# Kernel optimization log

Hardware: AMD Instinct MI355X
Metric: run time of the kernel (lower is better)

Reference implementation:

```python
import jax, jax.numpy as jnp
import numpy as np

NUM_GROUPS = 32
EPS = 1e-5


def group_norm(x, weight, bias):
    # x: (B, C, H, W, D); normalize per (group, spatial) per sample
    b, c, h, w, d = x.shape
    g = NUM_GROUPS
    xg = x.reshape(b, g, c // g, h, w, d)
    mean = xg.mean(axis=(2, 3, 4, 5), keepdims=True)
    var = xg.var(axis=(2, 3, 4, 5), keepdims=True)
    xg = (xg - mean) * jax.lax.rsqrt(var + EPS)
    xn = xg.reshape(b, c, h, w, d)
    return xn * weight[None, :, None, None, None] + bias[None, :, None, None, None]


def setup_inputs() -> dict:
    key = jax.random.key(0)
    ks = jax.random.split(key, 7)
    B, C, H, W, D = 4, 128, 16, 16, 16
    x = jax.random.normal(ks[0], (B, C, H, W, D), dtype=jnp.float32)
    gn_w = jnp.ones((C,), dtype=jnp.float32)
    gn_b = jnp.zeros((C,), dtype=jnp.float32)
    s = 1.0 / np.sqrt(C)
    qkv_w = jax.random.uniform(ks[1], (3 * C, C), minval=-s, maxval=s, dtype=jnp.float32)
    qkv_b = jax.random.uniform(ks[2], (3 * C,), minval=-s, maxval=s, dtype=jnp.float32)
    out_w = jax.random.uniform(ks[3], (C, C), minval=-s, maxval=s, dtype=jnp.float32)
    out_b = jax.random.uniform(ks[4], (C,), minval=-s, maxval=s, dtype=jnp.float32)
    return {"x": x, "gn_w": gn_w, "gn_b": gn_b, "qkv_w": qkv_w,
            "qkv_b": qkv_b, "out_w": out_w, "out_b": out_b}


def reference(x, gn_w, gn_b, qkv_w, qkv_b, out_w, out_b):
    b, c, h, w, d = x.shape
    n = h * w * d
    xn = group_norm(x, gn_w, gn_b)
    # 1x1x1 conv == pointwise linear over channels
    qkv = jnp.einsum('bchwd,oc->bohwd', xn, qkv_w) + qkv_b[None, :, None, None, None]
    q, k, v = jnp.split(qkv, 3, axis=1)
    q = q.transpose(0, 2, 3, 4, 1).reshape(b, n, c)   # (b, n, c)
    k = k.reshape(b, c, n)                             # (b, c, n)
    v = v.transpose(0, 2, 3, 4, 1).reshape(b, n, c)   # (b, n, c)
    scores = jnp.einsum('bnc,bcm->bnm', q, k) * (c ** -0.5)
    attn = jax.nn.softmax(scores, axis=-1)
    out = jnp.einsum('bnm,bmc->bnc', attn, v)          # (b, n, c)
    out = out.reshape(b, h, w, d, c).transpose(0, 4, 1, 2, 3)
    out = jnp.einsum('bchwd,oc->bohwd', out, out_w) + out_b[None, :, None, None, None]
    return out + x
```

## Files before the change

kernel.cpp:

```cpp
#include <hip/hip_runtime.h>

typedef unsigned short u16;
typedef __attribute__((ext_vector_type(8))) short bf16x8;
typedef __attribute__((ext_vector_type(4))) float f32x4;

__device__ __forceinline__ u16 f2bf(float f) {
    union { float f; unsigned u; } v; v.f = f;
    unsigned r = v.u + 0x7fffu + ((v.u >> 16) & 1u);
    return (u16)(r >> 16);
}

__device__ __forceinline__ void gload16(const u16* g, char* l) {
    __builtin_amdgcn_global_load_lds(
        (const __attribute__((address_space(1))) unsigned int*)g,
        (__attribute__((address_space(3))) unsigned int*)l, 16, 0, 0);
}

__global__ __launch_bounds__(256)
void k_stats(const float* __restrict__ x, float* __restrict__ mean, float* __restrict__ rstd)
{
    int bg = blockIdx.x, t = threadIdx.x;
    const float4* xp = (const float4*)(x + (size_t)bg * 16384);
    float s1 = 0.f, s2 = 0.f;
#pragma unroll
    for (int i = 0; i < 16; ++i) {
        float4 v = xp[i * 256 + t];
        s1 += v.x + v.y + v.z + v.w;
        s2 += v.x * v.x + v.y * v.y + v.z * v.z + v.w * v.w;
    }
#pragma unroll
    for (int off = 32; off >= 1; off >>= 1) {
        s1 += __shfl_xor(s1, off);
        s2 += __shfl_xor(s2, off);
    }
    __shared__ float a1[4], a2[4];
    if ((t & 63) == 0) { a1[t >> 6] = s1; a2[t >> 6] = s2; }
    __syncthreads();
    if (t == 0) {
        float t1 = a1[0] + a1[1] + a1[2] + a1[3];
        float t2 = a2[0] + a2[1] + a2[2] + a2[3];
        float mu = t1 * (1.f / 16384.f);
        float var = t2 * (1.f / 16384.f) - mu * mu;
        mean[bg] = mu;
        rstd[bg] = rsqrtf(var + 1e-5f);
    }
}

__global__ __launch_bounds__(384)
void k_qkv(const float* __restrict__ x, const float* __restrict__ gn_w, const float* __restrict__ gn_b,
           const float* __restrict__ qkv_w, const float* __restrict__ qkv_b,
           const float* __restrict__ mean, const float* __restrict__ rstd,
           u16* __restrict__ Qo, u16* __restrict__ Ko, u16* __restrict__ Vo)
{
    __shared__ float xn[128][64];
    int t = threadIdx.x;
    int b = blockIdx.x >> 6;
    int n0 = (blockIdx.x & 63) << 6;

    for (int e = t; e < 8192; e += 384) {
        int c = e >> 6, nn = e & 63;
        int bg = (b << 5) + (c >> 2);
        float sc = rstd[bg] * gn_w[c];
        float sh = gn_b[c] - mean[bg] * sc;
        xn[c][nn] = x[(size_t)(b * 128 + c) * 4096 + n0 + nn] * sc + sh;
    }
    __syncthreads();

    int o = t;
    float acc[64];
    float bias = qkv_b[o];
#pragma unroll
    for (int j = 0; j < 64; ++j) acc[j] = bias;

    const float4* wrow = (const float4*)(qkv_w + (size_t)o * 128);
    for (int c4 = 0; c4 < 32; ++c4) {
        float4 w4 = wrow[c4];
#pragma unroll
        for (int i = 0; i < 4; ++i) {
            int c = c4 * 4 + i;
            float wv = (i == 0) ? w4.x : (i == 1) ? w4.y : (i == 2) ? w4.z : w4.w;
#pragma unroll
            for (int j4 = 0; j4 < 16; ++j4) {
                float4 xv = *(const float4*)&xn[c][j4 * 4];
                acc[j4 * 4 + 0] = fmaf(xv.x, wv, acc[j4 * 4 + 0]);
                acc[j4 * 4 + 1] = fmaf(xv.y, wv, acc[j4 * 4 + 1]);
                acc[j4 * 4 + 2] = fmaf(xv.z, wv, acc[j4 * 4 + 2]);
                acc[j4 * 4 + 3] = fmaf(xv.w, wv, acc[j4 * 4 + 3]);
            }
        }
    }

    const float qscale = 0.08838834764831845f * 1.4426950408889634f;
    if (o < 128) {
        size_t base = (size_t)(b * 4096 + n0) * 128 + o;
#pragma unroll
        for (int nn = 0; nn < 64; ++nn) Qo[base + (size_t)nn * 128] = f2bf(acc[nn] * qscale);
    } else if (o < 256) {
        size_t base = (size_t)(b * 4096 + n0) * 128 + (o - 128);
#pragma unroll
        for (int nn = 0; nn < 64; ++nn) Ko[base + (size_t)nn * 128] = f2bf(acc[nn]);
    } else {
        size_t base = (size_t)(b * 128 + (o - 256)) * 4096 + n0;
#pragma unroll
        for (int g = 0; g < 8; ++g) {
            uint4 pk;
            pk.x = ((unsigned)f2bf(acc[g * 8 + 1]) << 16) | f2bf(acc[g * 8 + 0]);
            pk.y = ((unsigned)f2bf(acc[g * 8 + 3]) << 16) | f2bf(acc[g * 8 + 2]);
            pk.z = ((unsigned)f2bf(acc[g * 8 + 5]) << 16) | f2bf(acc[g * 8 + 4]);
            pk.w = ((unsigned)f2bf(acc[g * 8 + 7]) << 16) | f2bf(acc[g * 8 + 6]);
            *(uint4*)&Vo[base + g * 8] = pk;
        }
    }
}

__global__ __launch_bounds__(256, 2)
void k_attn(const u16* __restrict__ Qg, const u16* __restrict__ Kg, const u16* __restrict__ Vg,
            float* __restrict__ Opart, float* __restrict__ ml,
            int split, int kvlen, int iters)
{
    __shared__ __align__(16) u16 Kl[2][64 * 128];
    __shared__ __align__(16) u16 Vl[2][128 * 64];
    __shared__ __align__(16) u16 Pl[4 * 16 * 64];

    const int t = threadIdx.x;
    const int blk = blockIdx.x;
    const int half = blk % split;
    const int qt = (blk / split) & 63;
    const int b = blk / (split * 64);
    const int w = t >> 6;
    const int lane = t & 63;
    const int l15 = lane & 15;
    const int l4 = lane >> 4;
    const int q0 = qt << 6;
    const int swz = (l15 & 7) << 4;

    bf16x8 qf[4];
    {
        const u16* qb = Qg + (size_t)(b * 4096 + q0 + w * 16 + l15) * 128 + l4 * 8;
#pragma unroll
        for (int kc = 0; kc < 4; ++kc) qf[kc] = *(const bf16x8*)(qb + kc * 32);
    }
    f32x4 oac[8];
#pragma unroll
    for (int cf = 0; cf < 8; ++cf) oac[cf] = (f32x4){0.f, 0.f, 0.f, 0.f};
    float m = -__builtin_inff(), ls = 0.f;

    const int kv0 = half * kvlen;
    char* plw = (char*)Pl + w * 2048;

    const int krow = lane >> 4;
    const int vrow = lane >> 3;
    const int kcolA = ((lane & 15) ^ krow) * 8;
    const int kcolB = ((lane & 15) ^ (krow + 4)) * 8;
    const int vcol  = ((lane & 7) ^ (vrow & 7)) * 8;
    const u16* KgB = Kg + (size_t)b * 4096 * 128;
    const u16* VgB = Vg + (size_t)b * 128 * 4096;

    auto STAGE = [&](int buf, int kvb) {
        char* kd = (char*)&Kl[buf][0] + w * 4096;
        char* vd = (char*)&Vl[buf][0] + w * 4096;
        const u16* kga = KgB + (size_t)(kvb + 16 * w) * 128;
        const u16* vga = VgB + kvb + (size_t)(32 * w) * 4096;
#pragma unroll
        for (int i = 0; i < 4; ++i) {
            gload16(kga + (size_t)(4 * i + krow) * 128 + ((i & 1) ? kcolB : kcolA),
                    kd + i * 1024);
            gload16(vga + (size_t)(8 * i + vrow) * 4096 + vcol,
                    vd + i * 1024);
        }
    };

    STAGE(0, kv0);
    __syncthreads();

    int cur = 0;
    for (int it = 0; it < iters; ++it) {
        if (it + 1 < iters) STAGE(cur ^ 1, kv0 + (it + 1) * 64);

        const char* kb = (const char*)&Kl[cur][0];
        f32x4 st[4];
        __builtin_amdgcn_s_setprio(1);
#pragma unroll
        for (int mt = 0; mt < 4; ++mt) {
            f32x4 s = (f32x4){0.f, 0.f, 0.f, 0.f};
#pragma unroll
            for (int kc = 0; kc < 4; ++kc) {
                bf16x8 kf = *(const bf16x8*)(kb + (mt * 16 + l15) * 256 +
                                             ((kc * 64 + l4 * 16) ^ swz));
                s = __builtin_amdgcn_mfma_f32_16x16x32_bf16(kf, qf[kc], s, 0, 0, 0);
            }
            st[mt] = s;
        }
        __builtin_amdgcn_s_setprio(0);

        float pmax = -__builtin_inff();
#pragma unroll
        for (int mt = 0; mt < 4; ++mt)
            pmax = fmaxf(pmax, fmaxf(fmaxf(st[mt][0], st[mt][1]), fmaxf(st[mt][2], st[mt][3])));
        pmax = fmaxf(pmax, __shfl_xor(pmax, 16));
        pmax = fmaxf(pmax, __shfl_xor(pmax, 32));

        if (!__all(pmax - m <= 8.f)) {
            float nm = fmaxf(m, pmax);
            float fr = __builtin_amdgcn_exp2f(m - nm);
            m = nm;
            ls *= fr;
#pragma unroll
            for (int cf = 0; cf < 8; ++cf)
#pragma unroll
                for (int r = 0; r < 4; ++r) oac[cf][r] *= fr;
        }

        float rsum = 0.f;
        uint2 pw[4];
#pragma unroll
        for (int mt = 0; mt < 4; ++mt) {
            float p0 = __builtin_amdgcn_exp2f(st[mt][0] - m);
            float p1 = __builtin_amdgcn_exp2f(st[mt][1] - m);
            float p2 = __builtin_amdgcn_exp2f(st[mt][2] - m);
            float p3 = __builtin_amdgcn_exp2f(st[mt][3] - m);
            rsum += (p0 + p1) + (p2 + p3);
            pw[mt].x = ((unsigned)f2bf(p1) << 16) | f2bf(p0);
            pw[mt].y = ((unsigned)f2bf(p3) << 16) | f2bf(p2);
        }
        rsum += __shfl_xor(rsum, 16);
        rsum += __shfl_xor(rsum, 32);
        ls += rsum;

#pragma unroll
        for (int mt = 0; mt < 4; ++mt)
            *(uint2*)(plw + l15 * 128 + ((mt * 32 + l4 * 8) ^ swz)) = pw[mt];
        asm volatile("s_waitcnt lgkmcnt(0)" ::: "memory");
        __builtin_amdgcn_sched_barrier(0);

        const char* vb = (const char*)&Vl[cur][0];
        __builtin_amdgcn_s_setprio(1);
#pragma unroll
        for (int kc2 = 0; kc2 < 2; ++kc2) {
            bf16x8 pf = *(const bf16x8*)(plw + l15 * 128 + ((kc2 * 64 + l4 * 16) ^ swz));
#pragma unroll
            for (int cf = 0; cf < 8; ++cf) {
                bf16x8 vf = *(const bf16x8*)(vb + (cf * 16 + l15) * 128 +
                                             ((kc2 * 64 + l4 * 16) ^ swz));
                oac[cf] = __builtin_amdgcn_mfma_f32_16x16x32_bf16(vf, pf, oac[cf], 0, 0, 0);
            }
        }
        __builtin_amdgcn_s_setprio(0);
        __syncthreads();
        cur ^= 1;
    }

    {
        size_t qrow = ((size_t)half * 4 + b) * 4096 + q0 + w * 16 + l15;
        float* orow = Opart + qrow * 128;
#pragma unroll
        for (int cf = 0; cf < 8; ++cf) {
            float4 v;
            v.x = oac[cf][0]; v.y = oac[cf][1]; v.z = oac[cf][2]; v.w = oac[cf][3];
            *(float4*)&orow[cf * 16 + l4 * 4] = v;
        }
        if (l4 == 0) {
            size_t mb = (size_t)half * 16384 + b * 4096 + q0 + w * 16 + l15;
            ml[mb * 2 + 0] = m;
            ml[mb * 2 + 1] = ls;
        }
    }
}

__global__ __launch_bounds__(256)
void k_proj(const float* __restrict__ Opart, const float* __restrict__ ml,
            const float* __restrict__ x, const float* __restrict__ out_w,
            const float* __restrict__ out_b, float* __restrict__ out, int split)
{
    __shared__ float Ol[128][64];
    int t = threadIdx.x;
    int b = blockIdx.x >> 6;
    int n0 = (blockIdx.x & 63) << 6;

    for (int e = t; e < 2048; e += 256) {
        int nn = e >> 5, c4 = e & 31;
        size_t rg = (size_t)b * 4096 + n0 + nn;
        float msv[4], lsv[4];
#pragma unroll
        for (int s = 0; s < 4; ++s) {
            if (s < split) {
                msv[s] = ml[((size_t)s * 16384 + rg) * 2 + 0];
                lsv[s] = ml[((size_t)s * 16384 + rg) * 2 + 1];
            } else { msv[s] = -__builtin_inff(); lsv[s] = 0.f; }
        }
        float mm = fmaxf(fmaxf(msv[0], msv[1]), fmaxf(msv[2], msv[3]));
        float es[4]; float L = 0.f;
#pragma unroll
        for (int s = 0; s < 4; ++s) {
            es[s] = (s < split) ? __builtin_amdgcn_exp2f(msv[s] - mm) : 0.f;
            L += lsv[s] * es[s];
        }
        float inv = 1.f / L;
        float ox = 0.f, oy = 0.f, oz = 0.f, ow = 0.f;
#pragma unroll
        for (int s = 0; s < 4; ++s) {
            if (s < split) {
                float4 o4 = *(const float4*)&Opart[((size_t)s * 16384 + rg) * 128 + c4 * 4];
                ox = fmaf(o4.x, es[s], ox); oy = fmaf(o4.y, es[s], oy);
                oz = fmaf(o4.z, es[s], oz); ow = fmaf(o4.w, es[s], ow);
            }
        }
        Ol[c4 * 4 + 0][nn] = ox * inv;
        Ol[c4 * 4 + 1][nn] = oy * inv;
        Ol[c4 * 4 + 2][nn] = oz * inv;
        Ol[c4 * 4 + 3][nn] = ow * inv;
    }
    __syncthreads();

    int oc = t & 127, nh = t >> 7;
    float acc[32];
    float bias = out_b[oc];
#pragma unroll
    for (int j = 0; j < 32; ++j) acc[j] = bias;

    const float4* wrow = (const float4*)(out_w + (size_t)oc * 128);
    for (int c4 = 0; c4 < 32; ++c4) {
        float4 w4 = wrow[c4];
#pragma unroll
        for (int i = 0; i < 4; ++i) {
            int c = c4 * 4 + i;
            float wv = (i == 0) ? w4.x : (i == 1) ? w4.y : (i == 2) ? w4.z : w4.w;
#pragma unroll
            for (int j4 = 0; j4 < 8; ++j4) {
                float4 xv = *(const float4*)&Ol[c][nh * 32 + j4 * 4];
                acc[j4 * 4 + 0] = fmaf(xv.x, wv, acc[j4 * 4 + 0]);
                acc[j4 * 4 + 1] = fmaf(xv.y, wv, acc[j4 * 4 + 1]);
                acc[j4 * 4 + 2] = fmaf(xv.z, wv, acc[j4 * 4 + 2]);
                acc[j4 * 4 + 3] = fmaf(xv.w, wv, acc[j4 * 4 + 3]);
            }
        }
    }

    size_t ob = (size_t)(b * 128 + oc) * 4096 + n0 + nh * 32;
#pragma unroll
    for (int j4 = 0; j4 < 8; ++j4) {
        float4 xr = *(const float4*)&x[ob + j4 * 4];
        float4 ov;
        ov.x = acc[j4 * 4 + 0] + xr.x;
        ov.y = acc[j4 * 4 + 1] + xr.y;
        ov.z = acc[j4 * 4 + 2] + xr.z;
        ov.w = acc[j4 * 4 + 3] + xr.w;
        *(float4*)&out[ob + j4 * 4] = ov;
    }
}

extern "C" void kernel_launch(void* const* d_in, const int* in_sizes, int n_in,
                              void* d_out, int out_size, void* d_ws, size_t ws_size,
                              hipStream_t stream)
{
    const float* x     = (const float*)d_in[0];
    const float* gn_w  = (const float*)d_in[1];
    const float* gn_b  = (const float*)d_in[2];
    const float* qkv_w = (const float*)d_in[3];
    const float* qkv_b = (const float*)d_in[4];
    const float* out_w = (const float*)d_in[5];
    const float* out_b = (const float*)d_in[6];
    float* out = (float*)d_out;

    char* ws = (char*)d_ws;
    float* mean  = (float*)ws;
    float* rstd  = (float*)(ws + 512);
    u16*   Q     = (u16*)(ws + 4096);
    u16*   K     = (u16*)(ws + 4198400);
    u16*   V     = (u16*)(ws + 8392704);
    float* mlb   = (float*)(ws + 12587008);
    float* Opart = (float*)(ws + 13111296);

    int split = (ws_size >= (size_t)46700000) ? 4 : 2;
    int kvlen = 4096 / split;
    int iters = kvlen / 64;

    k_stats<<<128, 256, 0, stream>>>(x, mean, rstd);
    k_qkv<<<256, 384, 0, stream>>>(x, gn_w, gn_b, qkv_w, qkv_b, mean, rstd, Q, K, V);
    k_attn<<<256 * split, 256, 0, stream>>>(Q, K, V, Opart, mlb, split, kvlen, iters);
    k_proj<<<256, 256, 0, stream>>>(Opart, mlb, x, out_w, out_b, out, split);
}
```

Before: 157.3 us.

## Double query rows per attention wave and register-tile QKV/proj matmuls

Each attention wave now handles 32 query rows instead of 16, so every K and V fragment loaded from LDS feeds two MFMAs. This halves the grid and the K/V staging traffic per query. The QKV and output-projection kernels switch to 4x16 and 4x8 register tiles (four output channels per thread), which cuts LDS reads per FMA and makes Q/K stores wider. In exchange, register pressure in the attention kernel roughly doubles and fewer blocks are launched, which may lower occupancy and parallelism.

After: 126.9 us. -19.3%, faster.

```diff
diff --git a/kernel.cpp b/kernel.cpp
--- a/kernel.cpp
+++ b/kernel.cpp
@@ -66,49 +66,80 @@
     }
     __syncthreads();
 
-    int o = t;
-    float acc[64];
-    float bias = qkv_b[o];
-#pragma unroll
-    for (int j = 0; j < 64; ++j) acc[j] = bias;
-
-    const float4* wrow = (const float4*)(qkv_w + (size_t)o * 128);
+    const int og = t >> 2;
+    const int ng = t & 3;
+
+    float acc[4][16];
+#pragma unroll
+    for (int i = 0; i < 4; ++i) {
+        float bs = qkv_b[og * 4 + i];
+#pragma unroll
+        for (int j = 0; j < 16; ++j) acc[i][j] = bs;
+    }
+
+    const float4* wr0 = (const float4*)(qkv_w + (size_t)(og * 4 + 0) * 128);
+    const float4* wr1 = (const float4*)(qkv_w + (size_t)(og * 4 + 1) * 128);
+    const float4* wr2 = (const float4*)(qkv_w + (size_t)(og * 4 + 2) * 128);
+    const float4* wr3 = (const float4*)(qkv_w + (size_t)(og * 4 + 3) * 128);
+
     for (int c4 = 0; c4 < 32; ++c4) {
-        float4 w4 = wrow[c4];
+        float4 w0 = wr0[c4], w1 = wr1[c4], w2 = wr2[c4], w3 = wr3[c4];
+#pragma unroll
+        for (int cc = 0; cc < 4; ++cc) {
+            int c = c4 * 4 + cc;
+            float v0 = (cc == 0) ? w0.x : (cc == 1) ? w0.y : (cc == 2) ? w0.z : w0.w;
+            float v1 = (cc == 0) ? w1.x : (cc == 1) ? w1.y : (cc == 2) ? w1.z : w1.w;
+            float v2 = (cc == 0) ? w2.x : (cc == 1) ? w2.y : (cc == 2) ? w2.z : w2.w;
+            float v3 = (cc == 0) ? w3.x : (cc == 1) ? w3.y : (cc == 2) ? w3.z : w3.w;
+#pragma unroll
+            for (int j4 = 0; j4 < 4; ++j4) {
+                float4 xv = *(const float4*)&xn[c][ng * 16 + j4 * 4];
+#pragma unroll
+                for (int jj = 0; jj < 4; ++jj) {
+                    float xs = (jj == 0) ? xv.x : (jj == 1) ? xv.y : (jj == 2) ? xv.z : xv.w;
+                    acc[0][j4 * 4 + jj] = fmaf(xs, v0, acc[0][j4 * 4 + jj]);
+                    acc[1][j4 * 4 + jj] = fmaf(xs, v1, acc[1][j4 * 4 + jj]);
+                    acc[2][j4 * 4 + jj] = fmaf(xs, v2, acc[2][j4 * 4 + jj]);
+                    acc[3][j4 * 4 + jj] = fmaf(xs, v3, acc[3][j4 * 4 + jj]);
+                }
+            }
+        }
+    }
+
+    const float qscale = 0.08838834764831845f * 1.4426950408889634f;
+    if (og < 32) {
+        size_t base = (size_t)(b * 4096 + n0 + ng * 16) * 128 + og * 4;
+#pragma unroll
+        for (int n = 0; n < 16; ++n) {
+            uint2 pk;
+            pk.x = ((unsigned)f2bf(acc[1][n] * qscale) << 16) | f2bf(acc[0][n] * qscale);
+            pk.y = ((unsigned)f2bf(acc[3][n] * qscale) << 16) | f2bf(acc[2][n] * qscale);
+            *(uint2*)&Qo[base + (size_t)n * 128] = pk;
+        }
+    } else if (og < 64) {
+        size_t base = (size_t)(b * 4096 + n0 + ng * 16) * 128 + (og - 32) * 4;
+#pragma unroll
+        for (int n = 0; n < 16; ++n) {
+            uint2 pk;
+            pk.x = ((unsigned)f2bf(acc[1][n]) << 16) | f2bf(acc[0][n]);
+            pk.y = ((unsigned)f2bf(acc[3][n]) << 16) | f2bf(acc[2][n]);
+            *(uint2*)&Ko[base + (size_t)n * 128] = pk;
+        }
+    } else {
 #pragma unroll
         for (int i = 0; i < 4; ++i) {
-            int c = c4 * 4 + i;
-            float wv = (i == 0) ? w4.x : (i == 1) ? w4.y : (i == 2) ? w4.z : w4.w;
-#pragma unroll
-            for (int j4 = 0; j4 < 16; ++j4) {
-                float4 xv = *(const float4*)&xn[c][j4 * 4];
-                acc[j4 * 4 + 0] = fmaf(xv.x, wv, acc[j4 * 4 + 0]);
-                acc[j4 * 4 + 1] = fmaf(xv.y, wv, acc[j4 * 4 + 1]);
-                acc[j4 * 4 + 2] = fmaf(xv.z, wv, acc[j4 * 4 + 2]);
-                acc[j4 * 4 + 3] = fmaf(xv.w, wv, acc[j4 * 4 + 3]);
-            }
-        }
-    }
-
-    const float qscale = 0.08838834764831845f * 1.4426950408889634f;
-    if (o < 128) {
-        size_t base = (size_t)(b * 4096 + n0) * 128 + o;
-#pragma unroll
-        for (int nn = 0; nn < 64; ++nn) Qo[base + (size_t)nn * 128] = f2bf(acc[nn] * qscale);
-    } else if (o < 256) {
-        size_t base = (size_t)(b * 4096 + n0) * 128 + (o - 128);
-#pragma unroll
-        for (int nn = 0; nn < 64; ++nn) Ko[base + (size_t)nn * 128] = f2bf(acc[nn]);
-    } else {
-        size_t base = (size_t)(b * 128 + (o - 256)) * 4096 + n0;
-#pragma unroll
-        for (int g = 0; g < 8; ++g) {
-            uint4 pk;
-            pk.x = ((unsigned)f2bf(acc[g * 8 + 1]) << 16) | f2bf(acc[g * 8 + 0]);
-            pk.y = ((unsigned)f2bf(acc[g * 8 + 3]) << 16) | f2bf(acc[g * 8 + 2]);
-            pk.z = ((unsigned)f2bf(acc[g * 8 + 5]) << 16) | f2bf(acc[g * 8 + 4]);
-            pk.w = ((unsigned)f2bf(acc[g * 8 + 7]) << 16) | f2bf(acc[g * 8 + 6]);
-            *(uint4*)&Vo[base + g * 8] = pk;
+            size_t base = (size_t)(b * 128 + (og - 64) * 4 + i) * 4096 + n0 + ng * 16;
+            uint4 pa, pb;
+            pa.x = ((unsigned)f2bf(acc[i][1]) << 16) | f2bf(acc[i][0]);
+            pa.y = ((unsigned)f2bf(acc[i][3]) << 16) | f2bf(acc[i][2]);
+            pa.z = ((unsigned)f2bf(acc[i][5]) << 16) | f2bf(acc[i][4]);
+            pa.w = ((unsigned)f2bf(acc[i][7]) << 16) | f2bf(acc[i][6]);
+            pb.x = ((unsigned)f2bf(acc[i][9]) << 16) | f2bf(acc[i][8]);
+            pb.y = ((unsigned)f2bf(acc[i][11]) << 16) | f2bf(acc[i][10]);
+            pb.z = ((unsigned)f2bf(acc[i][13]) << 16) | f2bf(acc[i][12]);
+            pb.w = ((unsigned)f2bf(acc[i][15]) << 16) | f2bf(acc[i][14]);
+            *(uint4*)&Vo[base] = pa;
+            *(uint4*)&Vo[base + 8] = pb;
         }
     }
 }
@@ -120,33 +151,37 @@
 {
     __shared__ __align__(16) u16 Kl[2][64 * 128];
     __shared__ __align__(16) u16 Vl[2][128 * 64];
-    __shared__ __align__(16) u16 Pl[4 * 16 * 64];
+    __shared__ __align__(16) u16 Pl[4 * 32 * 64];
 
     const int t = threadIdx.x;
     const int blk = blockIdx.x;
     const int half = blk % split;
-    const int qt = (blk / split) & 63;
-    const int b = blk / (split * 64);
+    const int qt = (blk / split) & 31;
+    const int b = blk / (split * 32);
     const int w = t >> 6;
     const int lane = t & 63;
     const int l15 = lane & 15;
     const int l4 = lane >> 4;
-    const int q0 = qt << 6;
+    const int q0 = qt << 7;
     const int swz = (l15 & 7) << 4;
 
-    bf16x8 qf[4];
-    {
-        const u16* qb = Qg + (size_t)(b * 4096 + q0 + w * 16 + l15) * 128 + l4 * 8;
-#pragma unroll
-        for (int kc = 0; kc < 4; ++kc) qf[kc] = *(const bf16x8*)(qb + kc * 32);
-    }
-    f32x4 oac[8];
-#pragma unroll
-    for (int cf = 0; cf < 8; ++cf) oac[cf] = (f32x4){0.f, 0.f, 0.f, 0.f};
-    float m = -__builtin_inff(), ls = 0.f;
+    bf16x8 qf[2][4];
+#pragma unroll
+    for (int qh = 0; qh < 2; ++qh) {
+        const u16* qb = Qg + (size_t)(b * 4096 + q0 + w * 32 + qh * 16 + l15) * 128 + l4 * 8;
+#pragma unroll
+        for (int kc = 0; kc < 4; ++kc) qf[qh][kc] = *(const bf16x8*)(qb + kc * 32);
+    }
+    f32x4 oac[2][8];
+#pragma unroll
+    for (int qh = 0; qh < 2; ++qh)
+#pragma unroll
+        for (int cf = 0; cf < 8; ++cf) oac[qh][cf] = (f32x4){0.f, 0.f, 0.f, 0.f};
+    float m[2] = {-__builtin_inff(), -__builtin_inff()};
+    float lsum[2] = {0.f, 0.f};
 
     const int kv0 = half * kvlen;
-    char* plw = (char*)Pl + w * 2048;
+    char* plw = (char*)Pl + w * 4096;
 
     const int krow = lane >> 4;
     const int vrow = lane >> 3;
@@ -178,58 +213,65 @@
         if (it + 1 < iters) STAGE(cur ^ 1, kv0 + (it + 1) * 64);
 
         const char* kb = (const char*)&Kl[cur][0];
-        f32x4 st[4];
+        f32x4 st[2][4];
         __builtin_amdgcn_s_setprio(1);
 #pragma unroll
         for (int mt = 0; mt < 4; ++mt) {
-            f32x4 s = (f32x4){0.f, 0.f, 0.f, 0.f};
+            f32x4 s0 = (f32x4){0.f, 0.f, 0.f, 0.f};
+            f32x4 s1 = (f32x4){0.f, 0.f, 0.f, 0.f};
 #pragma unroll
             for (int kc = 0; kc < 4; ++kc) {
                 bf16x8 kf = *(const bf16x8*)(kb + (mt * 16 + l15) * 256 +
                                              ((kc * 64 + l4 * 16) ^ swz));
-                s = __builtin_amdgcn_mfma_f32_16x16x32_bf16(kf, qf[kc], s, 0, 0, 0);
-            }
-            st[mt] = s;
+                s0 = __builtin_amdgcn_mfma_f32_16x16x32_bf16(kf, qf[0][kc], s0, 0, 0, 0);
+                s1 = __builtin_amdgcn_mfma_f32_16x16x32_bf16(kf, qf[1][kc], s1, 0, 0, 0);
+            }
+            st[0][mt] = s0;
+            st[1][mt] = s1;
         }
         __builtin_amdgcn_s_setprio(0);
 
-        float pmax = -__builtin_inff();
-#pragma unroll
-        for (int mt = 0; mt < 4; ++mt)
-            pmax = fmaxf(pmax, fmaxf(fmaxf(st[mt][0], st[mt][1]), fmaxf(st[mt][2], st[mt][3])));
-        pmax = fmaxf(pmax, __shfl_xor(pmax, 16));
-        pmax = fmaxf(pmax, __shfl_xor(pmax, 32));
-
-        if (!__all(pmax - m <= 8.f)) {
-            float nm = fmaxf(m, pmax);
-            float fr = __builtin_amdgcn_exp2f(m - nm);
-            m = nm;
-            ls *= fr;
-#pragma unroll
-            for (int cf = 0; cf < 8; ++cf)
-#pragma unroll
-                for (int r = 0; r < 4; ++r) oac[cf][r] *= fr;
-        }
-
-        float rsum = 0.f;
-        uint2 pw[4];
-#pragma unroll
-        for (int mt = 0; mt < 4; ++mt) {
-            float p0 = __builtin_amdgcn_exp2f(st[mt][0] - m);
-            float p1 = __builtin_amdgcn_exp2f(st[mt][1] - m);
-            float p2 = __builtin_amdgcn_exp2f(st[mt][2] - m);
-            float p3 = __builtin_amdgcn_exp2f(st[mt][3] - m);
-            rsum += (p0 + p1) + (p2 + p3);
-            pw[mt].x = ((unsigned)f2bf(p1) << 16) | f2bf(p0);
-            pw[mt].y = ((unsigned)f2bf(p3) << 16) | f2bf(p2);
-        }
-        rsum += __shfl_xor(rsum, 16);
-        rsum += __shfl_xor(rsum, 32);
-        ls += rsum;
-
-#pragma unroll
-        for (int mt = 0; mt < 4; ++mt)
-            *(uint2*)(plw + l15 * 128 + ((mt * 32 + l4 * 8) ^ swz)) = pw[mt];
+#pragma unroll
+        for (int qh = 0; qh < 2; ++qh) {
+            float pmax = -__builtin_inff();
+#pragma unroll
+            for (int mt = 0; mt < 4; ++mt)
+                pmax = fmaxf(pmax, fmaxf(fmaxf(st[qh][mt][0], st[qh][mt][1]),
+                                         fmaxf(st[qh][mt][2], st[qh][mt][3])));
+            pmax = fmaxf(pmax, __shfl_xor(pmax, 16));
+            pmax = fmaxf(pmax, __shfl_xor(pmax, 32));
+
+            if (!__all(pmax - m[qh] <= 8.f)) {
+                float nm = fmaxf(m[qh], pmax);
+                float fr = __builtin_amdgcn_exp2f(m[qh] - nm);
+                m[qh] = nm;
+                lsum[qh] *= fr;
+#pragma unroll
+                for (int cf = 0; cf < 8; ++cf)
+#pragma unroll
+                    for (int r = 0; r < 4; ++r) oac[qh][cf][r] *= fr;
+            }
+
+            float rsum = 0.f;
+            uint2 pw[4];
+#pragma unroll
+            for (int mt = 0; mt < 4; ++mt) {
+                float p0 = __builtin_amdgcn_exp2f(st[qh][mt][0] - m[qh]);
+                float p1 = __builtin_amdgcn_exp2f(st[qh][mt][1] - m[qh]);
+                float p2 = __builtin_amdgcn_exp2f(st[qh][mt][2] - m[qh]);
+                float p3 = __builtin_amdgcn_exp2f(st[qh][mt][3] - m[qh]);
+                rsum += (p0 + p1) + (p2 + p3);
+                pw[mt].x = ((unsigned)f2bf(p1) << 16) | f2bf(p0);
+                pw[mt].y = ((unsigned)f2bf(p3) << 16) | f2bf(p2);
+            }
+            rsum += __shfl_xor(rsum, 16);
+            rsum += __shfl_xor(rsum, 32);
+            lsum[qh] += rsum;
+
+#pragma unroll
+            for (int mt = 0; mt < 4; ++mt)
+                *(uint2*)(plw + (qh * 16 + l15) * 128 + ((mt * 32 + l4 * 8) ^ swz)) = pw[mt];
+        }
         asm volatile("s_waitcnt lgkmcnt(0)" ::: "memory");
         __builtin_amdgcn_sched_barrier(0);
 
@@ -237,12 +279,14 @@
         __builtin_amdgcn_s_setprio(1);
 #pragma unroll
         for (int kc2 = 0; kc2 < 2; ++kc2) {
-            bf16x8 pf = *(const bf16x8*)(plw + l15 * 128 + ((kc2 * 64 + l4 * 16) ^ swz));
+            bf16x8 pf0 = *(const bf16x8*)(plw + (0 * 16 + l15) * 128 + ((kc2 * 64 + l4 * 16) ^ swz));
+            bf16x8 pf1 = *(const bf16x8*)(plw + (1 * 16 + l15) * 128 + ((kc2 * 64 + l4 * 16) ^ swz));
 #pragma unroll
             for (int cf = 0; cf < 8; ++cf) {
                 bf16x8 vf = *(const bf16x8*)(vb + (cf * 16 + l15) * 128 +
                                              ((kc2 * 64 + l4 * 16) ^ swz));
-                oac[cf] = __builtin_amdgcn_mfma_f32_16x16x32_bf16(vf, pf, oac[cf], 0, 0, 0);
+                oac[0][cf] = __builtin_amdgcn_mfma_f32_16x16x32_bf16(vf, pf0, oac[0][cf], 0, 0, 0);
+                oac[1][cf] = __builtin_amdgcn_mfma_f32_16x16x32_bf16(vf, pf1, oac[1][cf], 0, 0, 0);
             }
         }
         __builtin_amdgcn_s_setprio(0);
@@ -250,19 +294,21 @@
         cur ^= 1;
     }
 
-    {
-        size_t qrow = ((size_t)half * 4 + b) * 4096 + q0 + w * 16 + l15;
+#pragma unroll
+    for (int qh = 0; qh < 2; ++qh) {
+        size_t qrow = ((size_t)half * 4 + b) * 4096 + q0 + w * 32 + qh * 16 + l15;
         float* orow = Opart + qrow * 128;
 #pragma unroll
         for (int cf = 0; cf < 8; ++cf) {
             float4 v;
-            v.x = oac[cf][0]; v.y = oac[cf][1]; v.z = oac[cf][2]; v.w = oac[cf][3];
+            v.x = oac[qh][cf][0]; v.y = oac[qh][cf][1];
+            v.z = oac[qh][cf][2]; v.w = oac[qh][cf][3];
             *(float4*)&orow[cf * 16 + l4 * 4] = v;
         }
         if (l4 == 0) {
-            size_t mb = (size_t)half * 16384 + b * 4096 + q0 + w * 16 + l15;
-            ml[mb * 2 + 0] = m;
-            ml[mb * 2 + 1] = ls;
+            size_t mb = (size_t)half * 16384 + b * 4096 + q0 + w * 32 + qh * 16 + l15;
+            ml[mb * 2 + 0] = m[qh];
+            ml[mb * 2 + 1] = lsum[qh];
         }
     }
 }
@@ -312,40 +358,59 @@
     }
     __syncthreads();
 
-    int oc = t & 127, nh = t >> 7;
-    float acc[32];
-    float bias = out_b[oc];
-#pragma unroll
-    for (int j = 0; j < 32; ++j) acc[j] = bias;
-
-    const float4* wrow = (const float4*)(out_w + (size_t)oc * 128);
+    const int ocg = t & 31;
+    const int ng = t >> 5;
+
+    float acc[4][8];
+#pragma unroll
+    for (int i = 0; i < 4; ++i) {
+        float bs = out_b[ocg * 4 + i];
+#pragma unroll
+        for (int j = 0; j < 8; ++j) acc[i][j] = bs;
+    }
+
+    const float4* wr0 = (const float4*)(out_w + (size_t)(ocg * 4 + 0) * 128);
+    const float4* wr1 = (const float4*)(out_w + (size_t)(ocg * 4 + 1) * 128);
+    const float4* wr2 = (const float4*)(out_w + (size_t)(ocg * 4 + 2) * 128);
+    const float4* wr3 = (const float4*)(out_w + (size_t)(ocg * 4 + 3) * 128);
+
     for (int c4 = 0; c4 < 32; ++c4) {
-        float4 w4 = wrow[c4];
-#pragma unroll
-        for (int i = 0; i < 4; ++i) {
-            int c = c4 * 4 + i;
-            float wv = (i == 0) ? w4.x : (i == 1) ? w4.y : (i == 2) ? w4.z : w4.w;
-#pragma unroll
-            for (int j4 = 0; j4 < 8; ++j4) {
-                float4 xv = *(const float4*)&Ol[c][nh * 32 + j4 * 4];
-                acc[j4 * 4 + 0] = fmaf(xv.x, wv, acc[j4 * 4 + 0]);
-                acc[j4 * 4 + 1] = fmaf(xv.y, wv, acc[j4 * 4 + 1]);
-                acc[j4 * 4 + 2] = fmaf(xv.z, wv, acc[j4 * 4 + 2]);
-                acc[j4 * 4 + 3] = fmaf(xv.w, wv, acc[j4 * 4 + 3]);
-            }
-        }
-    }
-
-    size_t ob = (size_t)(b * 128 + oc) * 4096 + n0 + nh * 32;
-#pragma unroll
-    for (int j4 = 0; j4 < 8; ++j4) {
-        float4 xr = *(const float4*)&x[ob + j4 * 4];
-        float4 ov;
-        ov.x = acc[j4 * 4 + 0] + xr.x;
-        ov.y = acc[j4 * 4 + 1] + xr.y;
-        ov.z = acc[j4 * 4 + 2] + xr.z;
-        ov.w = acc[j4 * 4 + 3] + xr.w;
-        *(float4*)&out[ob + j4 * 4] = ov;
+        float4 w0 = wr0[c4], w1 = wr1[c4], w2 = wr2[c4], w3 = wr3[c4];
+#pragma unroll
+        for (int cc = 0; cc < 4; ++cc) {
+            int c = c4 * 4 + cc;
+            float v0 = (cc == 0) ? w0.x : (cc == 1) ? w0.y : (cc == 2) ? w0.z : w0.w;
+            float v1 = (cc == 0) ? w1.x : (cc == 1) ? w1.y : (cc == 2) ? w1.z : w1.w;
+            float v2 = (cc == 0) ? w2.x : (cc == 1) ? w2.y : (cc == 2) ? w2.z : w2.w;
+            float v3 = (cc == 0) ? w3.x : (cc == 1) ? w3.y : (cc == 2) ? w3.z : w3.w;
+#pragma unroll
+            for (int j4 = 0; j4 < 2; ++j4) {
+                float4 xv = *(const float4*)&Ol[c][ng * 8 + j4 * 4];
+#pragma unroll
+                for (int jj = 0; jj < 4; ++jj) {
+                    float xs = (jj == 0) ? xv.x : (jj == 1) ? xv.y : (jj == 2) ? xv.z : xv.w;
+                    acc[0][j4 * 4 + jj] = fmaf(xs, v0, acc[0][j4 * 4 + jj]);
+                    acc[1][j4 * 4 + jj] = fmaf(xs, v1, acc[1][j4 * 4 + jj]);
+                    acc[2][j4 * 4 + jj] = fmaf(xs, v2, acc[2][j4 * 4 + jj]);
+                    acc[3][j4 * 4 + jj] = fmaf(xs, v3, acc[3][j4 * 4 + jj]);
+                }
+            }
+        }
+    }
+
+#pragma unroll
+    for (int i = 0; i < 4; ++i) {
+        size_t ob = (size_t)(b * 128 + ocg * 4 + i) * 4096 + n0 + ng * 8;
+#pragma unroll
+        for (int j4 = 0; j4 < 2; ++j4) {
+            float4 xr = *(const float4*)&x[ob + j4 * 4];
+            float4 ov;
+            ov.x = acc[i][j4 * 4 + 0] + xr.x;
+            ov.y = acc[i][j4 * 4 + 1] + xr.y;
+            ov.z = acc[i][j4 * 4 + 2] + xr.z;
+            ov.w = acc[i][j4 * 4 + 3] + xr.w;
+            *(float4*)&out[ob + j4 * 4] = ov;
+        }
     }
 }
 
@@ -377,6 +442,6 @@
 
     k_stats<<<128, 256, 0, stream>>>(x, mean, rstd);
     k_qkv<<<256, 384, 0, stream>>>(x, gn_w, gn_b, qkv_w, qkv_b, mean, rstd, Q, K, V);
-    k_attn<<<256 * split, 256, 0, stream>>>(Q, K, V, Opart, mlb, split, kvlen, iters);
+    k_attn<<<128 * split, 256, 0, stream>>>(Q, K, V, Opart, mlb, split, kvlen, iters);
     k_proj<<<256, 256, 0, stream>>>(Opart, mlb, x, out_w, out_b, out, split);
 }
```
